# Kernel optimization log

Hardware: AMD Instinct MI355X
Metric: run time of the kernel (lower is better)

## Reference

```python
import jax, jax.numpy as jnp
import numpy as np

N = 100000      # nodes
E = 1600000     # edges
F_IN = 256      # num_features
H = 128         # hidden_dim
C = 16          # num_classes
LOG_SIGMA0 = float(np.log(0.1))  # prior_sigma = 0.1


def setup_inputs() -> dict:
    key = jax.random.key(0)
    ks = jax.random.split(key, 8)
    x = jax.random.normal(ks[0], (N, F_IN), jnp.float32)
    edge_index = jax.random.randint(ks[1], (2, E), 0, N, dtype=jnp.int64)
    # GCNConv linear weight + bias
    W = jax.random.normal(ks[2], (F_IN, H), jnp.float32) / np.float32(np.sqrt(F_IN))
    gcn_b = jnp.zeros((H,), jnp.float32)
    # BayesLinear params (mu + log_sigma) and fixed sampled noise eps
    w_mu = jax.random.normal(ks[3], (C, H), jnp.float32) / np.float32(np.sqrt(H))
    w_log_sigma = jnp.full((C, H), LOG_SIGMA0, jnp.float32)
    b_mu = jnp.zeros((C,), jnp.float32)
    b_log_sigma = jnp.full((C,), LOG_SIGMA0, jnp.float32)
    eps_w = jax.random.normal(ks[4], (C, H), jnp.float32)
    eps_b = jax.random.normal(ks[5], (C,), jnp.float32)
    return {"x": x, "edge_index": edge_index, "W": W, "gcn_b": gcn_b,
            "w_mu": w_mu, "w_log_sigma": w_log_sigma,
            "b_mu": b_mu, "b_log_sigma": b_log_sigma,
            "eps_w": eps_w, "eps_b": eps_b}


def reference(x, edge_index, W, gcn_b, w_mu, w_log_sigma, b_mu, b_log_sigma, eps_w, eps_b):
    n = x.shape[0]
    # --- GCNConv: add self-loops, symmetric deg^{-1/2} normalization ---
    loop = jnp.arange(n, dtype=edge_index.dtype)
    src = jnp.concatenate([edge_index[0], loop])  # message source j
    dst = jnp.concatenate([edge_index[1], loop])  # aggregation target i
    deg = jax.ops.segment_sum(jnp.ones_like(dst, dtype=x.dtype), dst, num_segments=n)
    deg_inv_sqrt = jnp.where(deg > 0, jax.lax.rsqrt(deg), 0.0)
    norm = deg_inv_sqrt[src] * deg_inv_sqrt[dst]            # [E+N]
    h = x @ W                                               # [N,H] transform first
    msg = h[src] * norm[:, None]                            # [E+N,H] gather
    agg = jax.ops.segment_sum(msg, dst, num_segments=n)     # [N,H] scatter-add
    agg = agg + gcn_b
    # --- ReLU; dropout is identity in eval mode ---
    a = jax.nn.relu(agg)
    # --- BayesLinear: w = mu + exp(log_sigma) * eps ---
    w = w_mu + jnp.exp(w_log_sigma) * eps_w                 # [C,H]
    b = b_mu + jnp.exp(b_log_sigma) * eps_b                 # [C]
    logits = a @ w.T + b                                    # [N,C]
    return jax.nn.log_softmax(logits, axis=1)
```

## Files before the change

kernel.cpp:

```cpp
#include <hip/hip_runtime.h>
#include <hip/hip_bf16.h>

#define N_NODES 100000
#define F_IN    256
#define H_DIM   128
#define C_CLS   16
#define NB_SCAN ((N_NODES + 255) / 256)
#define NSHARD  8
#define SHARD_W ((N_NODES + NSHARD - 1) / NSHARD)

typedef __attribute__((ext_vector_type(8))) short  short8;
typedef __attribute__((ext_vector_type(4))) float  float4v;
typedef __attribute__((ext_vector_type(4))) unsigned short ushort4v;

__device__ __forceinline__ float b2f(ushort u) {
    union { unsigned int i; float f; } v;
    v.i = ((unsigned int)u) << 16;
    return v.f;
}

__device__ __forceinline__ ushort f2b(float f) {
    unsigned int x = __float_as_uint(f);
    unsigned int r = (x + 0x7FFFu + ((x >> 16) & 1u)) >> 16;
    return (ushort)r;
}

__device__ __forceinline__ float ldsel(const void* p, int i, int f32f) {
    return f32f ? ((const float*)p)[i] : b2f(((const ushort*)p)[i]);
}

__global__ __launch_bounds__(64) void sniff(const ushort* __restrict__ x,
                                            const int* __restrict__ ei,
                                            int* __restrict__ flags) {
    int lane = threadIdx.x;
    int cnt_bf = 0;
#pragma unroll
    for (int j = 0; j < 4; ++j) {
        ushort u = x[lane * 4 + j];
        int e = (u >> 7) & 0xFF;
        if ((e >= 100 && e <= 140) || (u & 0x7FFF) == 0) cnt_bf++;
    }
    int zodd = (ei[2 * lane + 1] == 0) ? 1 : 0;
#pragma unroll
    for (int off = 32; off >= 1; off >>= 1) {
        cnt_bf += __shfl_xor(cnt_bf, off, 64);
        zodd   += __shfl_xor(zodd,   off, 64);
    }
    if (lane == 0) {
        flags[0] = (cnt_bf < 230) ? 1 : 0;
        flags[1] = (zodd  >= 32) ? 1 : 0;
    }
}

__global__ __launch_bounds__(256) void prep_params(const int* __restrict__ flags,
                                                   const void* __restrict__ W_any,
                                                   ushort* __restrict__ wtg,
                                                   const void* __restrict__ w_mu,
                                                   const void* __restrict__ w_ls,
                                                   const void* __restrict__ eps_w,
                                                   const void* __restrict__ b_mu,
                                                   const void* __restrict__ b_ls,
                                                   const void* __restrict__ eps_b,
                                                   const void* __restrict__ gcn_b,
                                                   ushort* __restrict__ whi,
                                                   ushort* __restrict__ wlo,
                                                   float* __restrict__ bias16,
                                                   float* __restrict__ gcnb_f) {
    const int f32f = flags[0];
    const int t = threadIdx.x;
    if (blockIdx.x < H_DIM) {
        const int n = blockIdx.x;
        float v = f32f ? ((const float*)W_any)[t * H_DIM + n]
                       : b2f(((const ushort*)W_any)[t * H_DIM + n]);
        wtg[n * F_IN + t] = f2b(v);
        return;
    }
#pragma unroll
    for (int i = t; i < C_CLS * H_DIM; i += 256) {
        float v = ldsel(w_mu, i, f32f) + __expf(ldsel(w_ls, i, f32f)) * ldsel(eps_w, i, f32f);
        ushort h = f2b(v);
        whi[i] = h;
        wlo[i] = f2b(v - b2f(h));
    }
    if (t < C_CLS)
        bias16[t] = ldsel(b_mu, t, f32f) + __expf(ldsel(b_ls, t, f32f)) * ldsel(eps_b, t, f32f);
    if (t < H_DIM)
        gcnb_f[t] = ldsel(gcn_b, t, f32f);
}

__global__ __launch_bounds__(256) void prep(const int* __restrict__ flags,
                                            const int* __restrict__ ei,
                                            int* __restrict__ cnt,
                                            int2* __restrict__ pr, int E) {
    int e = blockIdx.x * 256 + threadIdx.x;
    if (e >= E) return;
    int i64 = flags[1];
    int s = i64 ? ei[2L * e]          : ei[e];
    int d = i64 ? ei[2L * E + 2L * e] : ei[(long)E + e];
    pr[e] = make_int2(s, d);
    atomicAdd(&cnt[d], 1);
}

__global__ __launch_bounds__(256) void scan1(const int* __restrict__ cnt,
                                             int* __restrict__ offs,
                                             int* __restrict__ bsum) {
    __shared__ int sd[256];
    int t = threadIdx.x;
    int i = blockIdx.x * 256 + t;
    int v = (i < N_NODES) ? cnt[i] : 0;
    sd[t] = v;
    __syncthreads();
#pragma unroll
    for (int d = 1; d < 256; d <<= 1) {
        int add = (t >= d) ? sd[t - d] : 0;
        __syncthreads();
        sd[t] += add;
        __syncthreads();
    }
    if (i < N_NODES) offs[i] = sd[t] - v;
    if (t == 255) bsum[blockIdx.x] = sd[255];
}

__global__ __launch_bounds__(512) void scan2(const int* __restrict__ bsum,
                                             int* __restrict__ boff) {
    __shared__ int sd[512];
    int t = threadIdx.x;
    int v = (t < NB_SCAN) ? bsum[t] : 0;
    sd[t] = v;
    __syncthreads();
#pragma unroll
    for (int d = 1; d < 512; d <<= 1) {
        int add = (t >= d) ? sd[t - d] : 0;
        __syncthreads();
        sd[t] += add;
        __syncthreads();
    }
    if (t < NB_SCAN) boff[t] = sd[t] - v;
}

__global__ __launch_bounds__(256) void scan3(int* __restrict__ offs,
                                             const int* __restrict__ boff,
                                             const int* __restrict__ cnt,
                                             int* __restrict__ cursor,
                                             float* __restrict__ dis, int E) {
    int i = blockIdx.x * 256 + threadIdx.x;
    if (i == 0) offs[N_NODES] = E;
    if (i >= N_NODES) return;
    int off = offs[i] + boff[i >> 8];
    offs[i] = off;
    cursor[i] = off;
    dis[i] = rsqrtf((float)(cnt[i] + 1));
}

__global__ __launch_bounds__(256) void build_perm(const int2* __restrict__ pr,
                                                  int* __restrict__ cursor,
                                                  int* __restrict__ perm, int E) {
    const int shard = blockIdx.x & (NSHARD - 1);
    const int jb    = blockIdx.x >> 3;
    const int nb    = gridDim.x >> 3;
    const int lo = shard * SHARD_W;
    const int hi = lo + SHARD_W;
    for (int e = jb * 256 + threadIdx.x; e < E; e += nb * 256) {
        int2 p = pr[e];
        if (p.y >= lo && p.y < hi) {
            int slot = atomicAdd(&cursor[p.y], 1);
            perm[slot] = p.x;
        }
    }
}

__global__ __launch_bounds__(256) void gemm_xw(const int* __restrict__ flags,
                                               const void* __restrict__ x_any,
                                               const ushort* __restrict__ wtg,
                                               const float* __restrict__ dis,
                                               ushort* __restrict__ hout) {
    __shared__ __align__(16) ushort wt[128 * 128];
    const int f32f = flags[0];

    const int tid  = threadIdx.x;
    const int lane = tid & 63;
    const int quad = lane >> 4;
    const int lm   = lane & 15;
    const int wave = tid >> 6;

    const int rbase = blockIdx.x * 128 + wave * 32;
    int arow0 = rbase + lm;
    int arow1 = rbase + 16 + lm;
    if (arow0 >= N_NODES) arow0 = N_NODES - 1;
    if (arow1 >= N_NODES) arow1 = N_NODES - 1;
    const float*  xrf0 = (const float*) x_any + (size_t)arow0 * F_IN;
    const float*  xrf1 = (const float*) x_any + (size_t)arow1 * F_IN;
    const ushort* xrb0 = (const ushort*)x_any + (size_t)arow0 * F_IN;
    const ushort* xrb1 = (const ushort*)x_any + (size_t)arow1 * F_IN;

    float4v acc0[8], acc1[8];
#pragma unroll
    for (int c = 0; c < 8; ++c) {
        acc0[c] = (float4v){0.f, 0.f, 0.f, 0.f};
        acc1[c] = (float4v){0.f, 0.f, 0.f, 0.f};
    }

    for (int hh = 0; hh < 2; ++hh) {
        if (hh) __syncthreads();
#pragma unroll
        for (int it = 0; it < 8; ++it) {
            int flat = (it * 256 + tid) * 8;
            int col  = flat >> 7;
            int kloc = flat & 127;
            short8 v = *(const short8*)(wtg + col * F_IN + hh * 128 + kloc);
            int dst = ((col << 7) | kloc) ^ ((col & 7) << 3);
            *(short8*)(wt + dst) = v;
        }
        __syncthreads();
#pragma unroll
        for (int s = 0; s < 4; ++s) {
            int klocal = s * 32 + quad * 8;
            short8 afrag0, afrag1;
            if (f32f) {
                const float* p0 = xrf0 + hh * 128 + klocal;
                const float* p1 = xrf1 + hh * 128 + klocal;
                float4 u0 = *(const float4*)p0;
                float4 u1 = *(const float4*)(p0 + 4);
                float4 u2 = *(const float4*)p1;
                float4 u3 = *(const float4*)(p1 + 4);
                afrag0[0] = (short)f2b(u0.x); afrag0[1] = (short)f2b(u0.y);
                afrag0[2] = (short)f2b(u0.z); afrag0[3] = (short)f2b(u0.w);
                afrag0[4] = (short)f2b(u1.x); afrag0[5] = (short)f2b(u1.y);
                afrag0[6] = (short)f2b(u1.z); afrag0[7] = (short)f2b(u1.w);
                afrag1[0] = (short)f2b(u2.x); afrag1[1] = (short)f2b(u2.y);
                afrag1[2] = (short)f2b(u2.z); afrag1[3] = (short)f2b(u2.w);
                afrag1[4] = (short)f2b(u3.x); afrag1[5] = (short)f2b(u3.y);
                afrag1[6] = (short)f2b(u3.z); afrag1[7] = (short)f2b(u3.w);
            } else {
                afrag0 = *(const short8*)(xrb0 + hh * 128 + klocal);
                afrag1 = *(const short8*)(xrb1 + hh * 128 + klocal);
            }
#pragma unroll
            for (int c = 0; c < 8; ++c) {
                int colr = c * 16 + lm;
                int src = ((colr << 7) | klocal) ^ ((lm & 7) << 3);
                short8 bfrag = *(const short8*)(wt + src);
                acc0[c] = __builtin_amdgcn_mfma_f32_16x16x32_bf16(afrag0, bfrag, acc0[c], 0, 0, 0);
                acc1[c] = __builtin_amdgcn_mfma_f32_16x16x32_bf16(afrag1, bfrag, acc1[c], 0, 0, 0);
            }
        }
    }
    float dv0[4], dv1[4];
#pragma unroll
    for (int r = 0; r < 4; ++r) {
        int n0 = rbase + quad * 4 + r;
        int n1 = rbase + 16 + quad * 4 + r;
        dv0[r] = (n0 < N_NODES) ? dis[n0] : 0.f;
        dv1[r] = (n1 < N_NODES) ? dis[n1] : 0.f;
    }
#pragma unroll
    for (int c = 0; c < 8; ++c) {
        int col = c * 16 + lm;
#pragma unroll
        for (int r = 0; r < 4; ++r) {
            int n0 = rbase + quad * 4 + r;
            int n1 = rbase + 16 + quad * 4 + r;
            if (n0 < N_NODES) hout[(size_t)n0 * H_DIM + col] = f2b(acc0[c][r] * dv0[r]);
            if (n1 < N_NODES) hout[(size_t)n1 * H_DIM + col] = f2b(acc1[c][r] * dv1[r]);
        }
    }
}

__global__ __launch_bounds__(256) void gather_relu(const int* __restrict__ offs,
                                                   const int* __restrict__ perm,
                                                   const float* __restrict__ dis,
                                                   const ushort* __restrict__ hb,
                                                   const float* __restrict__ gcnb_f,
                                                   ushort* __restrict__ aout) {
    const int lane = threadIdx.x & 63;
    const int node = blockIdx.x * 4 + (threadIdx.x >> 6);
    if (node >= N_NODES) return;

    const int off0 = __builtin_amdgcn_readfirstlane(offs[node]);
    const int deg  = __builtin_amdgcn_readfirstlane(offs[node + 1]) - off0;
    const int* pp = perm + off0;

    float ax = 0.f, ay = 0.f;
    const int full = deg & ~15;
    for (int base = 0; base < full; base += 16) {
#pragma unroll
        for (int k = 0; k < 16; ++k) {
            int sk = pp[base + k];
            uint u = *((const uint*)(hb + (size_t)sk * H_DIM) + lane);
            ax += __uint_as_float(u << 16);
            ay += __uint_as_float(u & 0xFFFF0000u);
        }
    }
    {
        const int nb = deg - full;
#pragma unroll
        for (int k = 0; k < 16; ++k) {
            int   sk = 0;
            float wk = 0.f;
            if (k < nb) { sk = pp[full + k]; wk = 1.f; }
            uint u = *((const uint*)(hb + (size_t)sk * H_DIM) + lane);
            ax = fmaf(wk, __uint_as_float(u << 16),         ax);
            ay = fmaf(wk, __uint_as_float(u & 0xFFFF0000u), ay);
        }
    }

    const float dd = dis[node];
    uint us = *((const uint*)(hb + (size_t)node * H_DIM) + lane);
    float2 gb = *(const float2*)(gcnb_f + 2 * lane);
    ax = (ax + __uint_as_float(us << 16))         * dd + gb.x;
    ay = (ay + __uint_as_float(us & 0xFFFF0000u)) * dd + gb.y;
    ax = fmaxf(ax, 0.f);
    ay = fmaxf(ay, 0.f);
    uint pack = (uint)f2b(ax) | ((uint)f2b(ay) << 16);
    *((uint*)(aout + (size_t)node * H_DIM) + lane) = pack;
}

__global__ __launch_bounds__(256) void final_linear(const int* __restrict__ flags,
                                                    const ushort* __restrict__ a,
                                                    const ushort* __restrict__ whi,
                                                    const ushort* __restrict__ wlo,
                                                    const float* __restrict__ bias16,
                                                    void* __restrict__ out) {
    const int f32f = flags[0];
    const int lane = threadIdx.x & 63;
    const int wave = threadIdx.x >> 6;
    const int n0 = (blockIdx.x * 4 + wave) * 16;
    if (n0 >= N_NODES) return;
    const int lm = lane & 15, quad = lane >> 4;

    const ushort* arow = a   + (size_t)(n0 + lm) * H_DIM + quad * 8;
    const ushort* bh   = whi + lm * H_DIM + quad * 8;
    const ushort* bl   = wlo + lm * H_DIM + quad * 8;

    float4v acc = (float4v){0.f, 0.f, 0.f, 0.f};
#pragma unroll
    for (int s = 0; s < 4; ++s) {
        short8 af = *(const short8*)(arow + s * 32);
        short8 b0 = *(const short8*)(bh   + s * 32);
        short8 b1 = *(const short8*)(bl   + s * 32);
        acc = __builtin_amdgcn_mfma_f32_16x16x32_bf16(af, b0, acc, 0, 0, 0);
        acc = __builtin_amdgcn_mfma_f32_16x16x32_bf16(af, b1, acc, 0, 0, 0);
    }

    const float bias = bias16[lm];
    float p[4], m[4], ss[4];
#pragma unroll
    for (int r = 0; r < 4; ++r) { p[r] = acc[r] + bias; m[r] = p[r]; }
#pragma unroll
    for (int off = 1; off < 16; off <<= 1)
#pragma unroll
        for (int r = 0; r < 4; ++r) m[r] = fmaxf(m[r], __shfl_xor(m[r], off, 64));
#pragma unroll
    for (int r = 0; r < 4; ++r) ss[r] = __expf(p[r] - m[r]);
#pragma unroll
    for (int off = 1; off < 16; off <<= 1)
#pragma unroll
        for (int r = 0; r < 4; ++r) ss[r] += __shfl_xor(ss[r], off, 64);

    if (f32f) {
        float* op = (float*)out;
#pragma unroll
        for (int r = 0; r < 4; ++r)
            op[(size_t)(n0 + quad * 4 + r) * C_CLS + lm] = p[r] - m[r] - __logf(ss[r]);
    } else {
        ushort* op = (ushort*)out;
#pragma unroll
        for (int r = 0; r < 4; ++r)
            op[(size_t)(n0 + quad * 4 + r) * C_CLS + lm] = f2b(p[r] - m[r] - __logf(ss[r]));
    }
}

extern "C" void kernel_launch(void* const* d_in, const int* in_sizes, int n_in,
                              void* d_out, int out_size, void* d_ws, size_t ws_size,
                              hipStream_t stream) {
    const int E = in_sizes[1] / 2;

    char* wp = (char*)d_ws;
    auto alloc = [&](size_t bytes) -> char* {
        char* p = wp; wp += (bytes + 511) & ~(size_t)511; return p;
    };
    int*    flags  = (int*)   alloc(64);
    ushort* hb     = (ushort*)alloc((size_t)N_NODES * H_DIM * 2);
    ushort* aout   = (ushort*)alloc((size_t)N_NODES * H_DIM * 2);
    int*    cnt    = (int*)   alloc((size_t)N_NODES * 4);
    int*    offs   = (int*)   alloc((size_t)(N_NODES + 1) * 4);
    int*    cursor = (int*)   alloc((size_t)N_NODES * 4);
    int*    bsum   = (int*)   alloc((size_t)NB_SCAN * 4);
    int*    boff   = (int*)   alloc((size_t)NB_SCAN * 4);
    float*  dis    = (float*) alloc((size_t)N_NODES * 4);
    int*    perm   = (int*)   alloc((size_t)E * 4);
    int2*   pr     = (int2*)  alloc((size_t)E * 8);
    ushort* wtg    = (ushort*)alloc((size_t)H_DIM * F_IN * 2);
    ushort* whi    = (ushort*)alloc((size_t)C_CLS * H_DIM * 2);
    ushort* wlo    = (ushort*)alloc((size_t)C_CLS * H_DIM * 2);
    float*  bias16 = (float*) alloc((size_t)C_CLS * 4);
    float*  gcnb_f = (float*) alloc((size_t)H_DIM * 4);

    sniff<<<1, 64, 0, stream>>>((const ushort*)d_in[0], (const int*)d_in[1], flags);
    prep_params<<<H_DIM + 1, 256, 0, stream>>>(flags, d_in[2], wtg,
                                  d_in[4], d_in[5], d_in[8],
                                  d_in[6], d_in[7], d_in[9], d_in[3],
                                  whi, wlo, bias16, gcnb_f);
    (void)hipMemsetAsync(cnt, 0, (size_t)N_NODES * 4, stream);
    prep<<<(E + 255) / 256, 256, 0, stream>>>(flags, (const int*)d_in[1], cnt, pr, E);
    scan1<<<NB_SCAN, 256, 0, stream>>>(cnt, offs, bsum);
    scan2<<<1, 512, 0, stream>>>(bsum, boff);
    scan3<<<NB_SCAN, 256, 0, stream>>>(offs, boff, cnt, cursor, dis, E);
    build_perm<<<2048, 256, 0, stream>>>(pr, cursor, perm, E);
    gemm_xw<<<(N_NODES + 127) / 128, 256, 0, stream>>>(flags, d_in[0], wtg, dis, hb);
    gather_relu<<<(N_NODES + 3) / 4, 256, 0, stream>>>(offs, perm, dis, hb, gcnb_f, aout);
    final_linear<<<(N_NODES / C_CLS + 3) / 4, 256, 0, stream>>>(flags, aout, whi, wlo, bias16, (void*)d_out);
}
```

Measured before the change: 415.9 us.

## Bind build_perm shards to XCC id with atomic work-stealing chunk queues

Each block reads its hardware XCC id and first processes the destination shard mapped to that XCC. It pulls edge chunks from a per-shard atomic work counter, then steals from the other shards' queues once its own is exhausted. The intent is to keep the cursor atomics and perm writes for a node range local to one XCC's L2, which cuts cross-die coherence traffic, while balancing load dynamically. In exchange, every block now scans the whole edge list once per shard it joins, which adds global atomics and barriers per chunk and relies on the undocumented-in-code XCC register mapping.

```diff
diff --git a/kernel.cpp b/kernel.cpp
--- a/kernel.cpp
+++ b/kernel.cpp
@@ -8,6 +8,7 @@
 #define NB_SCAN ((N_NODES + 255) / 256)
 #define NSHARD  8
 #define SHARD_W ((N_NODES + NSHARD - 1) / NSHARD)
+#define CHUNK_E 4096
 
 typedef __attribute__((ext_vector_type(8))) short  short8;
 typedef __attribute__((ext_vector_type(4))) float  float4v;
@@ -154,17 +155,32 @@
 
 __global__ __launch_bounds__(256) void build_perm(const int2* __restrict__ pr,
                                                   int* __restrict__ cursor,
-                                                  int* __restrict__ perm, int E) {
-    const int shard = blockIdx.x & (NSHARD - 1);
-    const int jb    = blockIdx.x >> 3;
-    const int nb    = gridDim.x >> 3;
-    const int lo = shard * SHARD_W;
-    const int hi = lo + SHARD_W;
-    for (int e = jb * 256 + threadIdx.x; e < E; e += nb * 256) {
-        int2 p = pr[e];
-        if (p.y >= lo && p.y < hi) {
-            int slot = atomicAdd(&cursor[p.y], 1);
-            perm[slot] = p.x;
+                                                  int* __restrict__ perm,
+                                                  int* __restrict__ wc, int E) {
+    __shared__ int sbase;
+    unsigned xcc;
+    asm volatile("s_getreg_b32 %0, hwreg(HW_REG_XCC_ID)" : "=s"(xcc));
+    const int myshard = (int)(xcc & (NSHARD - 1));
+    const int t = threadIdx.x;
+
+    for (int r = 0; r < NSHARD; ++r) {
+        const int sh = (myshard + r) & (NSHARD - 1);
+        const int lo = sh * SHARD_W;
+        const int hi = lo + SHARD_W;
+        for (;;) {
+            if (t == 0) sbase = atomicAdd(&wc[sh], 1);
+            __syncthreads();
+            const long base = (long)sbase * CHUNK_E;
+            __syncthreads();
+            if (base >= E) break;
+            long end = base + CHUNK_E; if (end > E) end = E;
+            for (long e = base + t; e < end; e += 256) {
+                int2 p = pr[e];
+                if (p.y >= lo && p.y < hi) {
+                    int slot = atomicAdd(&cursor[p.y], 1);
+                    perm[slot] = p.x;
+                }
+            }
         }
     }
 }
@@ -390,6 +406,7 @@
     float*  dis    = (float*) alloc((size_t)N_NODES * 4);
     int*    perm   = (int*)   alloc((size_t)E * 4);
     int2*   pr     = (int2*)  alloc((size_t)E * 8);
+    int*    wc     = (int*)   alloc(64);
     ushort* wtg    = (ushort*)alloc((size_t)H_DIM * F_IN * 2);
     ushort* whi    = (ushort*)alloc((size_t)C_CLS * H_DIM * 2);
     ushort* wlo    = (ushort*)alloc((size_t)C_CLS * H_DIM * 2);
@@ -402,11 +419,12 @@
                                   d_in[6], d_in[7], d_in[9], d_in[3],
                                   whi, wlo, bias16, gcnb_f);
     (void)hipMemsetAsync(cnt, 0, (size_t)N_NODES * 4, stream);
+    (void)hipMemsetAsync(wc, 0, 64, stream);
     prep<<<(E + 255) / 256, 256, 0, stream>>>(flags, (const int*)d_in[1], cnt, pr, E);
     scan1<<<NB_SCAN, 256, 0, stream>>>(cnt, offs, bsum);
     scan2<<<1, 512, 0, stream>>>(bsum, boff);
     scan3<<<NB_SCAN, 256, 0, stream>>>(offs, boff, cnt, cursor, dis, E);
-    build_perm<<<2048, 256, 0, stream>>>(pr, cursor, perm, E);
+    build_perm<<<2048, 256, 0, stream>>>(pr, cursor, perm, wc, E);
     gemm_xw<<<(N_NODES + 127) / 128, 256, 0, stream>>>(flags, d_in[0], wtg, dis, hb);
     gather_relu<<<(N_NODES + 3) / 4, 256, 0, stream>>>(offs, perm, dis, hb, gcnb_f, aout);
     final_linear<<<(N_NODES / C_CLS + 3) / 4, 256, 0, stream>>>(flags, aout, whi, wlo, bias16, (void*)d_out);
```

New measurement: 609.5 us. +46.6%, slower.
